# Kernel optimization log

Measured on AMD Instinct MI355X. Metric: run time of the kernel, lower is better.

Reference implementation:

```python
import jax, jax.numpy as jnp
import numpy as np

B, T, P, I, H, O = 64, 32, 64, 256, 128, 88  # batch, time_steps, pitch_steps, input, hidden, output


def setup_inputs() -> dict:
    key = jax.random.key(0)
    ks = jax.random.split(key, 11)
    s = 0.05
    return {
        "x": jax.random.normal(ks[0], (B, T, P, I), jnp.float32),
        # stacked [fwd, bwd] direction weights, PyTorch LSTM gate order (i, f, g, o)
        "Wt_ih": jax.random.normal(ks[1], (2, 4 * H, I), jnp.float32) * s,
        "Wt_hh": jax.random.normal(ks[2], (2, 4 * H, H), jnp.float32) * s,
        "bt_ih": jax.random.normal(ks[3], (2, 4 * H), jnp.float32) * s,
        "bt_hh": jax.random.normal(ks[4], (2, 4 * H), jnp.float32) * s,
        "Wp_ih": jax.random.normal(ks[5], (2, 4 * H, 2 * H), jnp.float32) * s,
        "Wp_hh": jax.random.normal(ks[6], (2, 4 * H, H), jnp.float32) * s,
        "bp_ih": jax.random.normal(ks[7], (2, 4 * H), jnp.float32) * s,
        "bp_hh": jax.random.normal(ks[8], (2, 4 * H), jnp.float32) * s,
        "Wo": jax.random.normal(ks[9], (O, 2 * H), jnp.float32) * s,
        "bo": jax.random.normal(ks[10], (O,), jnp.float32) * s,
    }


def _cell(xt, h, c, Wih, Whh, bih, bhh):
    # PyTorch LSTMCell math, gate order i, f, g, o
    g = xt @ Wih.T + h @ Whh.T + bih + bhh  # [B, 4H]
    i, f, gc, o = jnp.split(g, 4, axis=-1)
    c2 = jax.nn.sigmoid(f) * c + jax.nn.sigmoid(i) * jnp.tanh(gc)
    h2 = jax.nn.sigmoid(o) * jnp.tanh(c2)
    return h2, c2


def reference(x, Wt_ih, Wt_hh, bt_ih, bt_hh, Wp_ih, Wp_hh, bp_ih, bp_hh, Wo, bo):
    b = x.shape[0]
    xs = x.reshape(b, T * P, I).transpose(1, 0, 2)  # [T*P, B, I] grid flattened in (t, p) order
    z = jnp.zeros((b, H), x.dtype)
    carry0 = (z, z, z, z, z, z, z, z)

    def step(carry, xt):
        htf, ctf, htb, ctb, hpf, cpf, hpb, cpb = carry
        # time LSTM: seq_len==1 so both directions see the same single step, state carried across grid
        htf, ctf = _cell(xt, htf, ctf, Wt_ih[0], Wt_hh[0], bt_ih[0], bt_hh[0])
        htb, ctb = _cell(xt, htb, ctb, Wt_ih[1], Wt_hh[1], bt_ih[1], bt_hh[1])
        tout = jnp.concatenate([htf, htb], axis=-1)  # [B, 2H]
        # pitch LSTM consumes time_out
        hpf, cpf = _cell(tout, hpf, cpf, Wp_ih[0], Wp_hh[0], bp_ih[0], bp_hh[0])
        hpb, cpb = _cell(tout, hpb, cpb, Wp_ih[1], Wp_hh[1], bp_ih[1], bp_hh[1])
        return (htf, ctf, htb, ctb, hpf, cpf, hpb, cpb), None

    carry, _ = jax.lax.scan(step, carry0, xs)
    pitch_out = jnp.concatenate([carry[4], carry[6]], axis=-1)  # last-step pitch output [B, 2H]
    return pitch_out @ Wo.T + bo  # [B, O]
```

## Files before the change

### kernel.cpp

```cpp
#include <hip/hip_runtime.h>
#include <hip/hip_fp16.h>
#include <stdint.h>


typedef _Float16 f16;
typedef _Float16 f16x4 __attribute__((ext_vector_type(4)));
typedef _Float16 f16x8 __attribute__((ext_vector_type(8)));
typedef float f32x4 __attribute__((ext_vector_type(4)));

#if defined(__has_builtin)
#if __has_builtin(__builtin_amdgcn_rcpf)
#define FRCP(x) __builtin_amdgcn_rcpf(x)
#else
#define FRCP(x) (1.f / (x))
#endif
#if __has_builtin(__builtin_amdgcn_exp2f)
#define FEXP2(x) __builtin_amdgcn_exp2f(x)
#else
#define FEXP2(x) __exp2f(x)
#endif
#endif

#define K_SIG 1.4426950409f
#define K_TANH 2.8853900818f

template <int CTRL>
static __device__ __forceinline__ float qperm(float v) {
    int r = __builtin_amdgcn_update_dpp(0, __builtin_bit_cast(int, v), CTRL, 0xf, 0xf, true);
    return __builtin_bit_cast(float, r);
}


__global__ __launch_bounds__(256) void k_convert_x(const float* __restrict__ x,
                                                   f16* __restrict__ xh) {
    size_t id = (size_t)blockIdx.x * 256 + threadIdx.x;
    const float4* src = (const float4*)(x + id * 8);
    float4 v0 = src[0], v1 = src[1];
    f16x8 o = {(f16)v0.x, (f16)v0.y, (f16)v0.z, (f16)v0.w,
               (f16)v1.x, (f16)v1.y, (f16)v1.z, (f16)v1.w};
    *(f16x8*)(xh + id * 8) = o;
}

__global__ __launch_bounds__(256) void k_convert_wp(const float* __restrict__ src,
                                                    f16* __restrict__ dst, int ksh, int n8) {
    int id = blockIdx.x * 256 + threadIdx.x;
    if (id >= n8) return;
    int rp = id >> ksh;
    int kb = id & ((1 << ksh) - 1);
    int dd = rp >> 9, gi = rp & 3, q = (rp >> 2) & 127;
    float sc = (gi == 2) ? K_TANH : -K_SIG;
    size_t so = ((size_t)(dd * 512 + gi * 128 + q) << (ksh + 3)) + kb * 8;
    const float4* sp = (const float4*)(src + so);
    float4 v0 = sp[0], v1 = sp[1];
    f16x8 o = {(f16)(v0.x * sc), (f16)(v0.y * sc), (f16)(v0.z * sc), (f16)(v0.w * sc),
               (f16)(v1.x * sc), (f16)(v1.y * sc), (f16)(v1.z * sc), (f16)(v1.w * sc)};
    *(f16x8*)(dst + (size_t)id * 8) = o;
}

__global__ __launch_bounds__(256) void k_bias(const float* __restrict__ a,
                                              const float* __restrict__ b,
                                              float* __restrict__ o) {
    int rp = blockIdx.x * 256 + threadIdx.x;
    int dd = rp >> 9, gi = rp & 3, q = (rp >> 2) & 127;
    int orig = dd * 512 + gi * 128 + q;
    float sc = (gi == 2) ? K_TANH : -K_SIG;
    o[rp] = (a[orig] + b[orig]) * sc;
}


#define BM 128
#define BN 128
#define BKK 32
#define LDT 40

__global__ __launch_bounds__(256) void k_gemm(const f16* __restrict__ A,
                                              const f16* __restrict__ B,
                                              f16* __restrict__ C,
                                              const float* __restrict__ bsum,
                                              int M, int N, int K) {
    __shared__ __align__(16) f16 As[BM * LDT];
    __shared__ __align__(16) f16 Bs[BN * LDT];
    const int tid  = threadIdx.x;
    const int m0   = blockIdx.x * BM;
    const int n0   = blockIdx.y * BN;
    const int lane = tid & 63;
    const int wave = tid >> 6;
    const int wm   = (wave & 1) * 64;
    const int wn   = (wave >> 1) * 64;
    const int r    = tid >> 1;
    const int koff = (tid & 1) * 16;
    const int mrow = lane & 15;
    const int kof  = (lane >> 4) * 8;
    const int crow = (lane >> 4) * 4;

    f32x4 acc[4][4];
#pragma unroll
    for (int i = 0; i < 4; ++i)
#pragma unroll
        for (int j = 0; j < 4; ++j) acc[i][j] = (f32x4){0.f, 0.f, 0.f, 0.f};

    for (int k0 = 0; k0 < K; k0 += BKK) {
        uint4 a0 = *(const uint4*)(A + (size_t)(m0 + r) * K + k0 + koff);
        uint4 a1 = *(const uint4*)(A + (size_t)(m0 + r) * K + k0 + koff + 8);
        uint4 b0 = *(const uint4*)(B + (size_t)(n0 + r) * K + k0 + koff);
        uint4 b1 = *(const uint4*)(B + (size_t)(n0 + r) * K + k0 + koff + 8);
        *(uint4*)(As + r * LDT + koff)     = a0;
        *(uint4*)(As + r * LDT + koff + 8) = a1;
        *(uint4*)(Bs + r * LDT + koff)     = b0;
        *(uint4*)(Bs + r * LDT + koff + 8) = b1;
        __syncthreads();
        f16x8 af[4], bfr[4];
#pragma unroll
        for (int i = 0; i < 4; ++i)
            af[i] = *(const f16x8*)(As + (wm + i * 16 + mrow) * LDT + kof);
#pragma unroll
        for (int j = 0; j < 4; ++j)
            bfr[j] = *(const f16x8*)(Bs + (wn + j * 16 + mrow) * LDT + kof);
#pragma unroll
        for (int i = 0; i < 4; ++i)
#pragma unroll
            for (int j = 0; j < 4; ++j)
                acc[i][j] = __builtin_amdgcn_mfma_f32_16x16x32_f16(af[i], bfr[j], acc[i][j], 0, 0, 0);
        __syncthreads();
    }
#pragma unroll
    for (int i = 0; i < 4; ++i) {
        const int rb = m0 + wm + i * 16 + crow;
        const float4 bbv = *(const float4*)(bsum + rb);
        const int dd = rb >> 9;
        const int uu = (rb & 511) >> 2;
#pragma unroll
        for (int j = 0; j < 4; ++j) {
            const int cm = n0 + wn + j * 16 + (lane & 15);
            const int b  = cm >> 11;
            const int s  = cm & 2047;
            f16x4 v = {(f16)(acc[i][j][0] + bbv.x), (f16)(acc[i][j][1] + bbv.y),
                       (f16)(acc[i][j][2] + bbv.z), (f16)(acc[i][j][3] + bbv.w)};
            size_t fofs = ((((size_t)b * 256 + (s >> 3)) * 2 + dd) * 128 + uu) * 32
                          + (s & 7) * 4;
            *(f16x4*)(C + fofs) = v;
        }
    }
}


template <int MODE>
__global__ void __attribute__((amdgpu_flat_work_group_size(512, 512),
                               amdgpu_waves_per_eu(2, 2))) k_lstm(
    const f16* __restrict__ G,
    const f16* __restrict__ Whh,
    f16* __restrict__ tout,
    float* __restrict__ hfin,
    const int S) {
    const int wg = blockIdx.x;
    const int b  = wg >> 1, d = wg & 1;
    const int t  = threadIdx.x;
    const int l  = t & 63, wv = t >> 6;
    const int hi = l >> 4, ch = l & 15;
    const int tt = ch >> 2, g = ch & 3;

    __shared__ __align__(16) f16 ring[16][128];

    f16x8 w[4][4];
#pragma unroll
    for (int q = 0; q < 4; ++q)
#pragma unroll
        for (int ks = 0; ks < 4; ++ks)
            w[q][ks] = *(const f16x8*)(Whh + ((size_t)d * 512 + (4 * wv + q) * 16 + ch) * 128
                                       + ks * 32 + hi * 8);

    for (int i = t; i < 1024; i += 512) ((uint32_t*)ring)[i] = 0;

    const int u = (4 * wv + tt) * 4 + hi;
    const f16* gp = G + ((((size_t)b * 256) * 2 + d) * 128 + u) * 32;

    const bool t0 = (tt & 1) != 0, t1 = (tt & 2) != 0;
    const bool r0 = (g & 1) != 0, r1 = (g & 2) != 0;
    const bool pG = (g & 2) != 0;
    const int  shG = (g & 1) * 16;
    const float Aact = (g == 2) ? 1.f : 0.f;
    const float Bact = (g == 2) ? -2.f : 1.f;
    const bool wrt = (g == 0);

    uint4 gc[4], gn[4];
#pragma unroll
    for (int q = 0; q < 4; ++q) gc[q] = *(const uint4*)(gp + q * 8);

    const f32x4 Z = {0.f, 0.f, 0.f, 0.f};
    float c = 0.f;
    __syncthreads();

    for (int sb = 0; sb < S; sb += 8) {
        {
            const size_t nb = (size_t)((sb + 8 < S) ? (sb >> 3) + 1 : (sb >> 3));
#pragma unroll
            for (int q = 0; q < 4; ++q) gn[q] = *(const uint4*)(gp + nb * 8192 + q * 8);
        }
        if (MODE == 1 && sb > 0 && t < 256) {
            const int jf = t >> 5, of = t & 31;
            uint2 hv = *(const uint2*)(&ring[((sb - 8) & 15) + jf][of * 4]);
            *(uint2*)(tout + ((size_t)b * 2048 + (sb - 8 + jf)) * 256 + d * 128 + of * 4) = hv;
        }
        const int half = sb & 15;
        const f16* rd0 = &ring[(half ^ 8) + 7][hi * 8];
        const f16* rdc = &ring[half][hi * 8];
        f16* wrp = &ring[half][u];
#pragma unroll
        for (int jj = 0; jj < 8; ++jj) {
            const int s = sb + jj;
            const f16* hb = (jj == 0) ? rd0 : (rdc + (jj - 1) * 128);
            f16x8 b0 = *(const f16x8*)(hb);
            f16x8 b1 = *(const f16x8*)(hb + 32);
            f16x8 b2 = *(const f16x8*)(hb + 64);
            f16x8 b3 = *(const f16x8*)(hb + 96);
            f32x4 A0 = __builtin_amdgcn_mfma_f32_16x16x32_f16(w[0][0], b0, Z, 0, 0, 0);
            f32x4 A1 = __builtin_amdgcn_mfma_f32_16x16x32_f16(w[1][0], b0, Z, 0, 0, 0);
            f32x4 A2 = __builtin_amdgcn_mfma_f32_16x16x32_f16(w[2][0], b0, Z, 0, 0, 0);
            f32x4 A3 = __builtin_amdgcn_mfma_f32_16x16x32_f16(w[3][0], b0, Z, 0, 0, 0);
            A0 = __builtin_amdgcn_mfma_f32_16x16x32_f16(w[0][1], b1, A0, 0, 0, 0);
            A1 = __builtin_amdgcn_mfma_f32_16x16x32_f16(w[1][1], b1, A1, 0, 0, 0);
            A2 = __builtin_amdgcn_mfma_f32_16x16x32_f16(w[2][1], b1, A2, 0, 0, 0);
            A3 = __builtin_amdgcn_mfma_f32_16x16x32_f16(w[3][1], b1, A3, 0, 0, 0);
            A0 = __builtin_amdgcn_mfma_f32_16x16x32_f16(w[0][2], b2, A0, 0, 0, 0);
            A1 = __builtin_amdgcn_mfma_f32_16x16x32_f16(w[1][2], b2, A1, 0, 0, 0);
            A2 = __builtin_amdgcn_mfma_f32_16x16x32_f16(w[2][2], b2, A2, 0, 0, 0);
            A3 = __builtin_amdgcn_mfma_f32_16x16x32_f16(w[3][2], b2, A3, 0, 0, 0);
            A0 = __builtin_amdgcn_mfma_f32_16x16x32_f16(w[0][3], b3, A0, 0, 0, 0);
            A1 = __builtin_amdgcn_mfma_f32_16x16x32_f16(w[1][3], b3, A1, 0, 0, 0);
            A2 = __builtin_amdgcn_mfma_f32_16x16x32_f16(w[2][3], b3, A2, 0, 0, 0);
            A3 = __builtin_amdgcn_mfma_f32_16x16x32_f16(w[3][3], b3, A3, 0, 0, 0);
            f32x4 X, Y, T;
#pragma unroll
            for (int e = 0; e < 4; ++e) {
                X[e] = t0 ? A1[e] : A0[e];
                Y[e] = t0 ? A3[e] : A2[e];
                T[e] = t1 ? Y[e] : X[e];
            }
            float xx = r0 ? T[1] : T[0];
            float yy = r0 ? T[3] : T[2];
            float v  = r1 ? yy : xx;
            uint32_t dw0 = (jj & 1) ? gc[jj >> 1].z : gc[jj >> 1].x;
            uint32_t dw1 = (jj & 1) ? gc[jj >> 1].w : gc[jj >> 1].y;
            uint32_t dsel = pG ? dw1 : dw0;
            v += (float)__builtin_bit_cast(f16, (uint16_t)(dsel >> shG));
            float wv_ = FRCP(1.f + FEXP2(v));
            float act = __builtin_fmaf(Bact, wv_, Aact);
            float gi = qperm<0x00>(act);
            float gf = qperm<0x55>(act);
            float gg = qperm<0xAA>(act);
            float go = qperm<0xFF>(act);
            c = __builtin_fmaf(gf, c, gi * gg);
            float tc = __builtin_fmaf(-2.f, FRCP(1.f + FEXP2(c * K_TANH)), 1.f);
            float hv = go * tc;
            if (wrt) *(wrp + jj * 128) = (f16)hv;
            if (MODE == 2 && s == S - 1 && wrt)
                hfin[(size_t)b * 256 + d * 128 + u] = hv;
            __asm__ __volatile__("s_waitcnt lgkmcnt(0)\n\ts_barrier" ::: "memory");
        }
#pragma unroll
        for (int q = 0; q < 4; ++q) gc[q] = gn[q];
    }
    if (MODE == 1 && t < 256) {
        const int jf = t >> 5, of = t & 31;
        uint2 hv = *(const uint2*)(&ring[((S - 8) & 15) + jf][of * 4]);
        *(uint2*)(tout + ((size_t)b * 2048 + (S - 8 + jf)) * 256 + d * 128 + of * 4) = hv;
    }
}


__global__ __launch_bounds__(128) void k_out(const float* __restrict__ hp,
                                             const float* __restrict__ Wo,
                                             const float* __restrict__ bo,
                                             float* __restrict__ out) {
    const int b = blockIdx.x;
    const int t = threadIdx.x;
    __shared__ float hs[256];
    hs[t] = hp[b * 256 + t];
    hs[t + 128] = hp[b * 256 + 128 + t];
    __syncthreads();
    if (t < 88) {
        float acc = bo[t];
        const float* wr = Wo + t * 256;
#pragma unroll 4
        for (int k = 0; k < 256; ++k) acc += wr[k] * hs[k];
        out[b * 88 + t] = acc;
    }
}


extern "C" void kernel_launch(void* const* d_in, const int* in_sizes, int n_in,
                              void* d_out, int out_size, void* d_ws, size_t ws_size,
                              hipStream_t stream) {
    const float* x    = (const float*)d_in[0];
    const float* Wtih = (const float*)d_in[1];
    const float* Wthh = (const float*)d_in[2];
    const float* btih = (const float*)d_in[3];
    const float* bthh = (const float*)d_in[4];
    const float* Wpih = (const float*)d_in[5];
    const float* Wphh = (const float*)d_in[6];
    const float* bpih = (const float*)d_in[7];
    const float* bphh = (const float*)d_in[8];
    const float* Wo   = (const float*)d_in[9];
    const float* bo   = (const float*)d_in[10];

    char* ws = (char*)d_ws;
    f16*   xh    = (f16*)(ws + 0);
    f16*   G     = (f16*)(ws + 67108864);
    f16*   tout  = (f16*)(ws + 335544320);
    f16*   wtih  = (f16*)(ws + 402653184);
    f16*   wthh  = (f16*)(ws + 403177472);
    f16*   wpih  = (f16*)(ws + 403439616);
    f16*   wphh  = (f16*)(ws + 403963904);
    float* bsT   = (float*)(ws + 404226048);
    float* bsP   = (float*)(ws + 404230144);
    float* hp    = (float*)(ws + 404226048);

    k_convert_x<<<16384, 256, 0, stream>>>(x, xh);
    k_convert_wp<<<128, 256, 0, stream>>>(Wtih, wtih, 5, 32768);
    k_convert_wp<<<64,  256, 0, stream>>>(Wthh, wthh, 4, 16384);
    k_convert_wp<<<128, 256, 0, stream>>>(Wpih, wpih, 5, 32768);
    k_convert_wp<<<64,  256, 0, stream>>>(Wphh, wphh, 4, 16384);
    k_bias<<<4, 256, 0, stream>>>(btih, bthh, bsT);
    k_bias<<<4, 256, 0, stream>>>(bpih, bphh, bsP);

    k_gemm<<<dim3(8, 1024), 256, 0, stream>>>(wtih, xh, G, bsT, 1024, 131072, 256);
    k_lstm<1><<<128, 512, 0, stream>>>(G, wthh, tout, nullptr, 2048);
    k_gemm<<<dim3(8, 1024), 256, 0, stream>>>(wpih, tout, G, bsP, 1024, 131072, 256);
    k_lstm<2><<<128, 512, 0, stream>>>(G, wphh, nullptr, hp, 2048);
    k_out<<<64, 128, 0, stream>>>(hp, Wo, bo, (float*)d_out);
}
```

Before: 2.359 ms.

## Halve LSTM workgroup to 4 waves, each wave computing two hidden-unit groups

The recurrent LSTM kernel now runs with 256 threads instead of 512. Each wave holds twice as many recurrent weight fragments in registers and computes two sets of gate outputs and cell states per step. The aim is to cut the per-step workgroup barrier cost, since fewer waves have to synchronize, and to give each wave more independent MFMA work to fill pipeline latency. The gate-preactivation layout written by the GEMM is changed to 4-step blocks so it matches the new prefetch pattern. The trade-off is higher register pressure and a longer serial MFMA chain per wave on every recurrent step.

```diff
diff --git a/kernel.cpp b/kernel.cpp
--- a/kernel.cpp
+++ b/kernel.cpp
@@ -136,8 +136,8 @@
             const int s  = cm & 2047;
             f16x4 v = {(f16)(acc[i][j][0] + bbv.x), (f16)(acc[i][j][1] + bbv.y),
                        (f16)(acc[i][j][2] + bbv.z), (f16)(acc[i][j][3] + bbv.w)};
-            size_t fofs = ((((size_t)b * 256 + (s >> 3)) * 2 + dd) * 128 + uu) * 32
-                          + (s & 7) * 4;
+            size_t fofs = ((((size_t)b * 512 + (s >> 2)) * 2 + dd) * 128 + uu) * 16
+                          + (s & 3) * 4;
             *(f16x4*)(C + fofs) = v;
         }
     }
@@ -145,8 +145,8 @@
 
 
 template <int MODE>
-__global__ void __attribute__((amdgpu_flat_work_group_size(512, 512),
-                               amdgpu_waves_per_eu(2, 2))) k_lstm(
+__global__ void __attribute__((amdgpu_flat_work_group_size(256, 256),
+                               amdgpu_waves_per_eu(1, 1))) k_lstm(
     const f16* __restrict__ G,
     const f16* __restrict__ Whh,
     f16* __restrict__ tout,
@@ -161,18 +161,20 @@
 
     __shared__ __align__(16) f16 ring[16][128];
 
-    f16x8 w[4][4];
-#pragma unroll
-    for (int q = 0; q < 4; ++q)
+    f16x8 w[8][4];
+#pragma unroll
+    for (int q = 0; q < 8; ++q)
 #pragma unroll
         for (int ks = 0; ks < 4; ++ks)
-            w[q][ks] = *(const f16x8*)(Whh + ((size_t)d * 512 + (4 * wv + q) * 16 + ch) * 128
+            w[q][ks] = *(const f16x8*)(Whh + ((size_t)d * 512 + (8 * wv + q) * 16 + ch) * 128
                                        + ks * 32 + hi * 8);
 
-    for (int i = t; i < 1024; i += 512) ((uint32_t*)ring)[i] = 0;
-
-    const int u = (4 * wv + tt) * 4 + hi;
-    const f16* gp = G + ((((size_t)b * 256) * 2 + d) * 128 + u) * 32;
+    for (int i = t; i < 1024; i += 256) ((uint32_t*)ring)[i] = 0;
+
+    const int u1 = (8 * wv + tt) * 4 + hi;
+    const int u2 = u1 + 16;
+    const f16* gp1 = G + (((size_t)b * 512 * 2 + d) * 128 + u1) * 16;
+    const f16* gp2 = gp1 + 16 * 16;
 
     const bool t0 = (tt & 1) != 0, t1 = (tt & 2) != 0;
     const bool r0 = (g & 1) != 0, r1 = (g & 2) != 0;
@@ -182,31 +184,38 @@
     const float Bact = (g == 2) ? -2.f : 1.f;
     const bool wrt = (g == 0);
 
-    uint4 gc[4], gn[4];
-#pragma unroll
-    for (int q = 0; q < 4; ++q) gc[q] = *(const uint4*)(gp + q * 8);
+    uint4 gc1[2], gn1[2], gc2[2], gn2[2];
+#pragma unroll
+    for (int k = 0; k < 2; ++k) {
+        gc1[k] = *(const uint4*)(gp1 + k * 8);
+        gc2[k] = *(const uint4*)(gp2 + k * 8);
+    }
 
     const f32x4 Z = {0.f, 0.f, 0.f, 0.f};
-    float c = 0.f;
+    float c1 = 0.f, c2 = 0.f;
     __syncthreads();
 
-    for (int sb = 0; sb < S; sb += 8) {
+    for (int sb = 0; sb < S; sb += 4) {
         {
-            const size_t nb = (size_t)((sb + 8 < S) ? (sb >> 3) + 1 : (sb >> 3));
-#pragma unroll
-            for (int q = 0; q < 4; ++q) gn[q] = *(const uint4*)(gp + nb * 8192 + q * 8);
+            const size_t nb = (size_t)((sb + 4 < S) ? (sb >> 2) + 1 : (sb >> 2));
+#pragma unroll
+            for (int k = 0; k < 2; ++k) {
+                gn1[k] = *(const uint4*)(gp1 + nb * 4096 + k * 8);
+                gn2[k] = *(const uint4*)(gp2 + nb * 4096 + k * 8);
+            }
         }
-        if (MODE == 1 && sb > 0 && t < 256) {
+        if (MODE == 1 && sb > 0 && t < 128) {
             const int jf = t >> 5, of = t & 31;
-            uint2 hv = *(const uint2*)(&ring[((sb - 8) & 15) + jf][of * 4]);
-            *(uint2*)(tout + ((size_t)b * 2048 + (sb - 8 + jf)) * 256 + d * 128 + of * 4) = hv;
+            uint2 hv = *(const uint2*)(&ring[((sb - 4) & 15) + jf][of * 4]);
+            *(uint2*)(tout + ((size_t)b * 2048 + (sb - 4 + jf)) * 256 + d * 128 + of * 4) = hv;
         }
         const int half = sb & 15;
-        const f16* rd0 = &ring[(half ^ 8) + 7][hi * 8];
+        const f16* rd0 = &ring[(half + 15) & 15][hi * 8];
         const f16* rdc = &ring[half][hi * 8];
-        f16* wrp = &ring[half][u];
-#pragma unroll
-        for (int jj = 0; jj < 8; ++jj) {
+        f16* wr1 = &ring[half][u1];
+        f16* wr2 = &ring[half][u2];
+#pragma unroll
+        for (int jj = 0; jj < 4; ++jj) {
             const int s = sb + jj;
             const f16* hb = (jj == 0) ? rd0 : (rdc + (jj - 1) * 128);
             f16x8 b0 = *(const f16x8*)(hb);
@@ -217,53 +226,98 @@
             f32x4 A1 = __builtin_amdgcn_mfma_f32_16x16x32_f16(w[1][0], b0, Z, 0, 0, 0);
             f32x4 A2 = __builtin_amdgcn_mfma_f32_16x16x32_f16(w[2][0], b0, Z, 0, 0, 0);
             f32x4 A3 = __builtin_amdgcn_mfma_f32_16x16x32_f16(w[3][0], b0, Z, 0, 0, 0);
+            f32x4 A4 = __builtin_amdgcn_mfma_f32_16x16x32_f16(w[4][0], b0, Z, 0, 0, 0);
+            f32x4 A5 = __builtin_amdgcn_mfma_f32_16x16x32_f16(w[5][0], b0, Z, 0, 0, 0);
+            f32x4 A6 = __builtin_amdgcn_mfma_f32_16x16x32_f16(w[6][0], b0, Z, 0, 0, 0);
+            f32x4 A7 = __builtin_amdgcn_mfma_f32_16x16x32_f16(w[7][0], b0, Z, 0, 0, 0);
             A0 = __builtin_amdgcn_mfma_f32_16x16x32_f16(w[0][1], b1, A0, 0, 0, 0);
             A1 = __builtin_amdgcn_mfma_f32_16x16x32_f16(w[1][1], b1, A1, 0, 0, 0);
             A2 = __builtin_amdgcn_mfma_f32_16x16x32_f16(w[2][1], b1, A2, 0, 0, 0);
             A3 = __builtin_amdgcn_mfma_f32_16x16x32_f16(w[3][1], b1, A3, 0, 0, 0);
+            A4 = __builtin_amdgcn_mfma_f32_16x16x32_f16(w[4][1], b1, A4, 0, 0, 0);
+            A5 = __builtin_amdgcn_mfma_f32_16x16x32_f16(w[5][1], b1, A5, 0, 0, 0);
+            A6 = __builtin_amdgcn_mfma_f32_16x16x32_f16(w[6][1], b1, A6, 0, 0, 0);
+            A7 = __builtin_amdgcn_mfma_f32_16x16x32_f16(w[7][1], b1, A7, 0, 0, 0);
             A0 = __builtin_amdgcn_mfma_f32_16x16x32_f16(w[0][2], b2, A0, 0, 0, 0);
             A1 = __builtin_amdgcn_mfma_f32_16x16x32_f16(w[1][2], b2, A1, 0, 0, 0);
             A2 = __builtin_amdgcn_mfma_f32_16x16x32_f16(w[2][2], b2, A2, 0, 0, 0);
             A3 = __builtin_amdgcn_mfma_f32_16x16x32_f16(w[3][2], b2, A3, 0, 0, 0);
+            A4 = __builtin_amdgcn_mfma_f32_16x16x32_f16(w[4][2], b2, A4, 0, 0, 0);
+            A5 = __builtin_amdgcn_mfma_f32_16x16x32_f16(w[5][2], b2, A5, 0, 0, 0);
+            A6 = __builtin_amdgcn_mfma_f32_16x16x32_f16(w[6][2], b2, A6, 0, 0, 0);
+            A7 = __builtin_amdgcn_mfma_f32_16x16x32_f16(w[7][2], b2, A7, 0, 0, 0);
             A0 = __builtin_amdgcn_mfma_f32_16x16x32_f16(w[0][3], b3, A0, 0, 0, 0);
             A1 = __builtin_amdgcn_mfma_f32_16x16x32_f16(w[1][3], b3, A1, 0, 0, 0);
             A2 = __builtin_amdgcn_mfma_f32_16x16x32_f16(w[2][3], b3, A2, 0, 0, 0);
             A3 = __builtin_amdgcn_mfma_f32_16x16x32_f16(w[3][3], b3, A3, 0, 0, 0);
-            f32x4 X, Y, T;
-#pragma unroll
-            for (int e = 0; e < 4; ++e) {
-                X[e] = t0 ? A1[e] : A0[e];
-                Y[e] = t0 ? A3[e] : A2[e];
-                T[e] = t1 ? Y[e] : X[e];
-            }
-            float xx = r0 ? T[1] : T[0];
-            float yy = r0 ? T[3] : T[2];
-            float v  = r1 ? yy : xx;
-            uint32_t dw0 = (jj & 1) ? gc[jj >> 1].z : gc[jj >> 1].x;
-            uint32_t dw1 = (jj & 1) ? gc[jj >> 1].w : gc[jj >> 1].y;
-            uint32_t dsel = pG ? dw1 : dw0;
-            v += (float)__builtin_bit_cast(f16, (uint16_t)(dsel >> shG));
-            float wv_ = FRCP(1.f + FEXP2(v));
-            float act = __builtin_fmaf(Bact, wv_, Aact);
-            float gi = qperm<0x00>(act);
-            float gf = qperm<0x55>(act);
-            float gg = qperm<0xAA>(act);
-            float go = qperm<0xFF>(act);
-            c = __builtin_fmaf(gf, c, gi * gg);
-            float tc = __builtin_fmaf(-2.f, FRCP(1.f + FEXP2(c * K_TANH)), 1.f);
-            float hv = go * tc;
-            if (wrt) *(wrp + jj * 128) = (f16)hv;
-            if (MODE == 2 && s == S - 1 && wrt)
-                hfin[(size_t)b * 256 + d * 128 + u] = hv;
+            A4 = __builtin_amdgcn_mfma_f32_16x16x32_f16(w[4][3], b3, A4, 0, 0, 0);
+            A5 = __builtin_amdgcn_mfma_f32_16x16x32_f16(w[5][3], b3, A5, 0, 0, 0);
+            A6 = __builtin_amdgcn_mfma_f32_16x16x32_f16(w[6][3], b3, A6, 0, 0, 0);
+            A7 = __builtin_amdgcn_mfma_f32_16x16x32_f16(w[7][3], b3, A7, 0, 0, 0);
+            float v1, v2;
+            {
+                f32x4 X, Y, T;
+#pragma unroll
+                for (int e = 0; e < 4; ++e) {
+                    X[e] = t0 ? A1[e] : A0[e];
+                    Y[e] = t0 ? A3[e] : A2[e];
+                    T[e] = t1 ? Y[e] : X[e];
+                }
+                float xx = r0 ? T[1] : T[0];
+                float yy = r0 ? T[3] : T[2];
+                v1 = r1 ? yy : xx;
+            }
+            {
+                f32x4 X, Y, T;
+#pragma unroll
+                for (int e = 0; e < 4; ++e) {
+                    X[e] = t0 ? A5[e] : A4[e];
+                    Y[e] = t0 ? A7[e] : A6[e];
+                    T[e] = t1 ? Y[e] : X[e];
+                }
+                float xx = r0 ? T[1] : T[0];
+                float yy = r0 ? T[3] : T[2];
+                v2 = r1 ? yy : xx;
+            }
+            {
+                uint32_t dwA1 = (jj & 1) ? gc1[jj >> 1].z : gc1[jj >> 1].x;
+                uint32_t dwB1 = (jj & 1) ? gc1[jj >> 1].w : gc1[jj >> 1].y;
+                uint32_t ds1 = pG ? dwB1 : dwA1;
+                v1 += (float)__builtin_bit_cast(f16, (uint16_t)(ds1 >> shG));
+                uint32_t dwA2 = (jj & 1) ? gc2[jj >> 1].z : gc2[jj >> 1].x;
+                uint32_t dwB2 = (jj & 1) ? gc2[jj >> 1].w : gc2[jj >> 1].y;
+                uint32_t ds2 = pG ? dwB2 : dwA2;
+                v2 += (float)__builtin_bit_cast(f16, (uint16_t)(ds2 >> shG));
+            }
+            float act1 = __builtin_fmaf(Bact, FRCP(1.f + FEXP2(v1)), Aact);
+            float act2 = __builtin_fmaf(Bact, FRCP(1.f + FEXP2(v2)), Aact);
+            float gi1 = qperm<0x00>(act1), gi2 = qperm<0x00>(act2);
+            float gf1 = qperm<0x55>(act1), gf2 = qperm<0x55>(act2);
+            float gg1 = qperm<0xAA>(act1), gg2 = qperm<0xAA>(act2);
+            float go1 = qperm<0xFF>(act1), go2 = qperm<0xFF>(act2);
+            c1 = __builtin_fmaf(gf1, c1, gi1 * gg1);
+            c2 = __builtin_fmaf(gf2, c2, gi2 * gg2);
+            float tc1 = __builtin_fmaf(-2.f, FRCP(1.f + FEXP2(c1 * K_TANH)), 1.f);
+            float tc2 = __builtin_fmaf(-2.f, FRCP(1.f + FEXP2(c2 * K_TANH)), 1.f);
+            float h1 = go1 * tc1;
+            float h2 = go2 * tc2;
+            if (wrt) {
+                *(wr1 + jj * 128) = (f16)h1;
+                *(wr2 + jj * 128) = (f16)h2;
+            }
+            if (MODE == 2 && s == S - 1 && wrt) {
+                hfin[(size_t)b * 256 + d * 128 + u1] = h1;
+                hfin[(size_t)b * 256 + d * 128 + u2] = h2;
+            }
             __asm__ __volatile__("s_waitcnt lgkmcnt(0)\n\ts_barrier" ::: "memory");
         }
 #pragma unroll
-        for (int q = 0; q < 4; ++q) gc[q] = gn[q];
-    }
-    if (MODE == 1 && t < 256) {
+        for (int k = 0; k < 2; ++k) { gc1[k] = gn1[k]; gc2[k] = gn2[k]; }
+    }
+    if (MODE == 1 && t < 128) {
         const int jf = t >> 5, of = t & 31;
-        uint2 hv = *(const uint2*)(&ring[((S - 8) & 15) + jf][of * 4]);
-        *(uint2*)(tout + ((size_t)b * 2048 + (S - 8 + jf)) * 256 + d * 128 + of * 4) = hv;
+        uint2 hv = *(const uint2*)(&ring[((S - 4) & 15) + jf][of * 4]);
+        *(uint2*)(tout + ((size_t)b * 2048 + (S - 4 + jf)) * 256 + d * 128 + of * 4) = hv;
     }
 }
 
@@ -324,8 +378,8 @@
     k_bias<<<4, 256, 0, stream>>>(bpih, bphh, bsP);
 
     k_gemm<<<dim3(8, 1024), 256, 0, stream>>>(wtih, xh, G, bsT, 1024, 131072, 256);
-    k_lstm<1><<<128, 512, 0, stream>>>(G, wthh, tout, nullptr, 2048);
+    k_lstm<1><<<128, 256, 0, stream>>>(G, wthh, tout, nullptr, 2048);
     k_gemm<<<dim3(8, 1024), 256, 0, stream>>>(wpih, tout, G, bsP, 1024, 131072, 256);
-    k_lstm<2><<<128, 512, 0, stream>>>(G, wphh, nullptr, hp, 2048);
+    k_lstm<2><<<128, 256, 0, stream>>>(G, wphh, nullptr, hp, 2048);
     k_out<<<64, 128, 0, stream>>>(hp, Wo, bo, (float*)d_out);
 }
```

Result: slower. 2.809 ms (+19.1%).
